# Kernel optimization log

Hardware: AMD Instinct MI355X
Metric: run time of the kernel (lower is better)

Reference implementation:

```python
import jax, jax.numpy as jnp
import numpy as np

NUM_IMU = 72
NUM_NOISE = 12
MAX_PROP = 300
LN_EPS = 1e-5

def _softplus(x):
    return jax.nn.softplus(x)

def setup_inputs() -> dict:
    key = jax.random.key(0)
    k1, k2, k3, k4, k5 = jax.random.split(key, 5)
    d_model = 1024
    seq_len = 4096
    hidden_states = jax.random.normal(k1, (1, seq_len, d_model), dtype=jnp.float32)
    ln_gamma = jnp.ones((d_model,), dtype=jnp.float32)
    ln_beta = jnp.zeros((d_model,), dtype=jnp.float32)
    # Linear: d_model -> NUM_IMU * NUM_NOISE
    W = jax.random.normal(k2, (d_model, NUM_IMU * NUM_NOISE), dtype=jnp.float32) / np.sqrt(d_model)
    b = jax.random.normal(k3, (NUM_IMU * NUM_NOISE,), dtype=jnp.float32) * 0.01
    return {"hidden_states": hidden_states, "ln_gamma": ln_gamma, "ln_beta": ln_beta, "W": W, "b": b}

def _forward(hidden_states, ln_gamma, ln_beta, W, b):
    seq_len = hidden_states.shape[1]
    tsteps = min(MAX_PROP, seq_len)
    x = hidden_states[0]  # [seq, d_model] (squeeze batch=1)
    mu = jnp.mean(x, axis=-1, keepdims=True)
    var = jnp.mean((x - mu) ** 2, axis=-1, keepdims=True)
    xn = (x - mu) * jax.lax.rsqrt(var + LN_EPS) * ln_gamma + ln_beta
    # noise params: [seq, NUM_NOISE, NUM_IMU]
    p = (xn @ W + b).reshape(seq_len, NUM_NOISE, NUM_IMU)
    c = p[:, 4, :]
    c_theta = p[:, 5, :]
    phi = p[:, 6, :]
    phi_theta = p[:, 7, :]
    d = _softplus(p[:, 1, :])
    k = d ** 2 / 4 + _softplus(p[:, 0, :])
    d_theta = _softplus(p[:, 3, :])
    k_theta = d_theta ** 2 / 4 + _softplus(p[:, 2, :])
    acc_base = p[:, 8, :].T      # [imu, seq]
    acc_std = _softplus(p[:, 9, :]).T
    gyro_base = p[:, 10, :].T
    gyro_std = _softplus(p[:, 11, :]).T
    # vectorize over imu: move to [imu, seq, 1]
    def I(a):
        return a.T[:, :, None]
    t = jnp.arange(tsteps, dtype=jnp.float32)[None, None, :]  # [1,1,tstep]
    k_, d_, phi_, c_ = I(k), I(d), I(phi), I(c)
    kt_, dt_, pht_, ct_ = I(k_theta), I(d_theta), I(phi_theta), I(c_theta)
    omega1 = jnp.sqrt(k_ * 4 - d_ ** 2) / 2
    lin = c_ * jnp.exp(-d_ / 2 * t) * jnp.sin(t * omega1 + phi_)
    omega2 = jnp.sqrt(kt_ * 4 - dt_ ** 2) / 2
    ang = ct_ * jnp.exp(-dt_ / 2 * t) * jnp.sin(t * omega2 + pht_)
    spring = lin + ang  # [imu, seq, tstep]
    # banded scatter-add: out[s+t] += spring[:, s, t] for s+t < seq_len
    pos = jnp.arange(seq_len, dtype=jnp.int32)[:, None] + jnp.arange(tsteps, dtype=jnp.int32)[None, :]
    pos_flat = pos.reshape(-1)
    mask = pos_flat < seq_len
    pos_safe = jnp.where(mask, pos_flat, 0)
    vals = spring.reshape(NUM_IMU, -1) * mask.astype(spring.dtype)
    kinematics = jnp.zeros((NUM_IMU, seq_len), dtype=spring.dtype).at[:, pos_safe].add(vals)
    return kinematics, acc_base, acc_std, gyro_base, gyro_std

def reference(hidden_states, ln_gamma, ln_beta, W, b):
    return _forward(hidden_states, ln_gamma, ln_beta, W, b)
```

## Files before the change

### kernel.cpp

```cpp
#include <hip/hip_runtime.h>
#include <hip/hip_bf16.h>
#include <math.h>

#define SEQ 4096
#define DM  1024
#define NIMU 72
#define NNOISE 12
#define NJ (NIMU*NNOISE)
#define TSTEPS 300
#define PLANE (NIMU*SEQ)

#define A2F_SHORTS ((size_t)256 * 64 * 512)
#define BTF_SHORTS ((size_t)56 * 64 * 512)

typedef __attribute__((ext_vector_type(8))) short bf16x8;
typedef __attribute__((ext_vector_type(4))) float f32x4;
typedef __attribute__((ext_vector_type(2))) float f32x2;

__device__ __forceinline__ float softplus_f(float x) {
    return fmaxf(x, 0.f) + log1pf(expf(-fabsf(x)));
}

__device__ __forceinline__ void split_bf16(float x, short& hi, short& lo) {
    unsigned b = __float_as_uint(x);
    unsigned h = (b + 0x7FFFu + ((b >> 16) & 1u)) >> 16;
    float hf = __uint_as_float(h << 16);
    float r = x - hf;
    unsigned b2 = __float_as_uint(r);
    unsigned l2 = (b2 + 0x7FFFu + ((b2 >> 16) & 1u)) >> 16;
    hi = (short)h;
    lo = (short)l2;
}

__global__ __launch_bounds__(256) void ln_kernel(const float* __restrict__ x,
                                                 const float* __restrict__ gamma,
                                                 const float* __restrict__ beta,
                                                 short* __restrict__ A2f) {
    const int s_tile = blockIdx.x;
    const int tid = threadIdx.x;
    const int mrow = tid >> 4;
    const int g    = tid & 15;
    const int row  = s_tile * 16 + mrow;
    const float4* xr = (const float4*)(x + (size_t)row * DM);

    float s = 0.f, sq = 0.f;
    #pragma unroll
    for (int i = 0; i < 16; ++i) {
        float4 v = xr[g + 16 * i];
        s  += v.x + v.y + v.z + v.w;
        sq += v.x*v.x + v.y*v.y + v.z*v.z + v.w*v.w;
    }
    #pragma unroll
    for (int off = 1; off < 16; off <<= 1) {
        s  += __shfl_xor(s, off);
        sq += __shfl_xor(sq, off);
    }
    const float mean = s * (1.f / DM);
    const float var  = sq * (1.f / DM) - mean * mean;
    const float rstd = rsqrtf(fmaxf(var, 0.f) + 1e-5f);

    #pragma unroll
    for (int i = 0; i < 16; ++i) {
        float4 v = xr[g + 16 * i];
        float4 gm = ((const float4*)gamma)[g + 16 * i];
        float4 bt = ((const float4*)beta)[g + 16 * i];
        float o[4];
        o[0] = (v.x - mean) * rstd * gm.x + bt.x;
        o[1] = (v.y - mean) * rstd * gm.y + bt.y;
        o[2] = (v.z - mean) * rstd * gm.z + bt.z;
        o[3] = (v.w - mean) * rstd * gm.w + bt.w;
        short4 hv, lv;
        split_bf16(o[0], hv.x, lv.x);
        split_bf16(o[1], hv.y, lv.y);
        split_bf16(o[2], hv.z, lv.z);
        split_bf16(o[3], hv.w, lv.w);
        const int ch = (g >> 3) + 2 * i;
        const size_t base = ((size_t)s_tile * 64 + ch) * 512
                          + mrow * 8 + ((g >> 1) & 3) * 128 + (g & 1) * 4;
        *(short4*)(A2f + base)             = hv;
        *(short4*)(A2f + base + 32 * 512)  = lv;
    }
}

__global__ __launch_bounds__(256) void wprep_kernel(const float* __restrict__ W,
                                                    short* __restrict__ Btf) {
    __shared__ float T[32][33];
    const int k0 = blockIdx.x * 32, j0 = blockIdx.y * 32;
    const int t = threadIdx.x;
    {
        const int r = t >> 3, c4 = (t & 7) * 4;
        float4 v = *(const float4*)(W + (size_t)(k0 + r) * NJ + j0 + c4);
        T[r][c4 + 0] = v.x; T[r][c4 + 1] = v.y; T[r][c4 + 2] = v.z; T[r][c4 + 3] = v.w;
    }
    __syncthreads();
    if (t < 128) {
        const int gq = t >> 6;
        const int l  = t & 63;
        const int n = l & 15, c = l >> 4;
        const int jt = blockIdx.y * 2 + gq;
        bf16x8 hv, lv;
        #pragma unroll
        for (int o = 0; o < 8; ++o) {
            short h, lo_;
            split_bf16(T[c * 8 + o][gq * 16 + n], h, lo_);
            hv[o] = h; lv[o] = lo_;
        }
        short* dh = Btf + ((size_t)jt * 64 + blockIdx.x) * 512 + l * 8;
        *(bf16x8*)dh = hv;
        *(bf16x8*)(dh + (size_t)32 * 512) = lv;
    }
}

__global__ __launch_bounds__(256, 1) void gemm_kernel(const short* __restrict__ A2f,
                                                      const short* __restrict__ Btf,
                                                      const float* __restrict__ bias,
                                                      float* __restrict__ pt) {
    const int l = threadIdx.x & 63, w = threadIdx.x >> 6;
    const int st0 = blockIdx.x * 8 + (w & 1) * 4;
    const int jt0 = blockIdx.y * 8 + (w >> 1) * 4;
    const short* aB = A2f + (size_t)st0 * (64 * 512) + l * 8;
    const short* bB = Btf + (size_t)jt0 * (64 * 512) + l * 8;

    f32x4 acc[4][4] = {};
    bf16x8 ah[2][4], al[2][4], bh[2][4], bl[2][4];

    auto ldstep = [&](int slot, int i) {
        #pragma unroll
        for (int t = 0; t < 4; ++t) {
            ah[slot][t] = *(const bf16x8*)(aB + ((size_t)t * 64 + i) * 512);
            al[slot][t] = *(const bf16x8*)(aB + ((size_t)t * 64 + 32 + i) * 512);
            bh[slot][t] = *(const bf16x8*)(bB + ((size_t)t * 64 + i) * 512);
            bl[slot][t] = *(const bf16x8*)(bB + ((size_t)t * 64 + 32 + i) * 512);
        }
    };

    ldstep(0, 0);
    #pragma unroll 2
    for (int i = 0; i < 32; ++i) {
        const int cur = i & 1;
        if (i + 1 < 32) ldstep(cur ^ 1, i + 1);
        #pragma unroll
        for (int mi = 0; mi < 4; ++mi)
            #pragma unroll
            for (int ni = 0; ni < 4; ++ni)
                acc[mi][ni] = __builtin_amdgcn_mfma_f32_16x16x32_bf16(
                    ah[cur][mi], bh[cur][ni], acc[mi][ni], 0, 0, 0);
        #pragma unroll
        for (int mi = 0; mi < 4; ++mi)
            #pragma unroll
            for (int ni = 0; ni < 4; ++ni)
                acc[mi][ni] = __builtin_amdgcn_mfma_f32_16x16x32_bf16(
                    ah[cur][mi], bl[cur][ni], acc[mi][ni], 0, 0, 0);
        #pragma unroll
        for (int mi = 0; mi < 4; ++mi)
            #pragma unroll
            for (int ni = 0; ni < 4; ++ni)
                acc[mi][ni] = __builtin_amdgcn_mfma_f32_16x16x32_bf16(
                    al[cur][mi], bh[cur][ni], acc[mi][ni], 0, 0, 0);
    }

    const int srow = (l >> 4) * 4;
    const int jcol = l & 15;
    #pragma unroll
    for (int ni = 0; ni < 4; ++ni) {
        const int j = (jt0 + ni) * 16 + jcol;
        if (j < NJ) {
            const float bj = bias[j];
            #pragma unroll
            for (int mi = 0; mi < 4; ++mi) {
                f32x4 v = acc[mi][ni];
                v[0] += bj; v[1] += bj; v[2] += bj; v[3] += bj;
                *(f32x4*)(pt + (size_t)j * SEQ + (st0 + mi) * 16 + srow) = v;
            }
        }
    }
}

__global__ __launch_bounds__(256) void spring_kernel(const float* __restrict__ pt,
                                                     float* __restrict__ kin) {
    __shared__ float win[4 * 368];
    const int tid  = threadIdx.x;
    const int lane = tid & 63;
    const int wid  = tid >> 6;
    const int s0   = blockIdx.x * 256;
    const int imu  = blockIdx.y;
    const int s    = s0 + (wid << 6) + lane;

    float* w0 = win + wid * 368;
    #pragma unroll
    for (int i = 0; i < 6; ++i) {
        const int idx = lane + i * 64;
        if (idx < 363) w0[idx] = 0.f;
    }

    const int base = imu * SEQ + s;
    const float p0  = pt[(size_t)0 * PLANE + base];
    const float p1  = pt[(size_t)1 * PLANE + base];
    const float p2  = pt[(size_t)2 * PLANE + base];
    const float p3  = pt[(size_t)3 * PLANE + base];
    const float c1  = pt[(size_t)4 * PLANE + base];
    const float c2  = pt[(size_t)5 * PLANE + base];
    const float ph1 = pt[(size_t)6 * PLANE + base];
    const float ph2 = pt[(size_t)7 * PLANE + base];

    float dd = softplus_f(p1);
    float kk = dd * dd * 0.25f + softplus_f(p0);
    float om1 = 0.5f * sqrtf(fmaxf(4.f * kk - dd * dd, 0.f));
    float dt = softplus_f(p3);
    float kt = dt * dt * 0.25f + softplus_f(p2);
    float om2 = 0.5f * sqrtf(fmaxf(4.f * kt - dt * dt, 0.f));
    float e1 = expf(-0.5f * dd), e2 = expf(-0.5f * dt);
    float sn, cs, sn2, cs2;
    sincosf(om1, &sn, &cs);
    sincosf(om2, &sn2, &cs2);
    f32x2 Rr = {e1 * cs, e2 * cs2};
    f32x2 Ri = {e1 * sn, e2 * sn2};
    sincosf(ph1, &sn, &cs);
    sincosf(ph2, &sn2, &cs2);
    f32x2 zr = {c1 * cs, c2 * cs2};
    f32x2 zi = {c1 * sn, c2 * sn2};

    f32x2 zrB, ziB;
    {
        f32x2 prr = Rr, pri = Ri;
        f32x2 qr = {1.f, 1.f}, qi = {0.f, 0.f};
        int e = 150;
        while (e) {
            if (e & 1) {
                f32x2 nr = qr * prr - qi * pri;
                qi = qr * pri + qi * prr;
                qr = nr;
            }
            f32x2 nr = prr * prr - pri * pri;
            pri = 2.f * prr * pri;
            prr = nr;
            e >>= 1;
        }
        f32x2 nr = zr * qr - zi * qi;
        ziB = zr * qi + zi * qr;
        zrB = nr;
    }

    float* wp = w0 + lane;
    #pragma unroll 1
    for (int tb = 0; tb < 128; tb += 32) {
        float* wq = wp + tb;
        #pragma unroll
        for (int j = 0; j < 32; ++j) {
            const float vA = zi.x + zi.y;
            const float vB = ziB.x + ziB.y;
            const float a = wq[j];
            const float b = wq[j + 150];
            wq[j]       = a + vA;
            wq[j + 150] = b + vB;
            f32x2 nr = zr * Rr - zi * Ri;
            zi = zr * Ri + zi * Rr;
            zr = nr;
            nr = zrB * Rr - ziB * Ri;
            ziB = zrB * Ri + ziB * Rr;
            zrB = nr;
            __asm__ volatile("" ::: "memory");
        }
    }
    {
        float* wq = wp + 128;
        #pragma unroll
        for (int j = 0; j < 22; ++j) {
            const float vA = zi.x + zi.y;
            const float vB = ziB.x + ziB.y;
            const float a = wq[j];
            const float b = wq[j + 150];
            wq[j]       = a + vA;
            wq[j + 150] = b + vB;
            f32x2 nr = zr * Rr - zi * Ri;
            zi = zr * Ri + zi * Rr;
            zr = nr;
            nr = zrB * Rr - ziB * Ri;
            ziB = zrB * Ri + ziB * Rr;
            zrB = nr;
            __asm__ volatile("" ::: "memory");
        }
    }

    __syncthreads();
    for (int i = tid; i < 555; i += 256) {
        float sum = 0.f;
        #pragma unroll
        for (int w = 0; w < 4; ++w) {
            const int idx = i - (w << 6);
            if (idx >= 0 && idx < 363) sum += win[w * 368 + idx];
        }
        const int pos = s0 + i;
        if (pos < SEQ) {
            (void)__hip_atomic_fetch_add(&kin[(size_t)imu * SEQ + pos], sum,
                                         __ATOMIC_RELAXED, __HIP_MEMORY_SCOPE_AGENT);
        }
    }
}

__global__ __launch_bounds__(256) void tail_kernel(const float* __restrict__ pt,
                                                   float* __restrict__ out) {
    int idx = blockIdx.x * 256 + threadIdx.x;
    if (idx >= 4 * PLANE) return;
    float v = pt[(size_t)8 * PLANE + idx];
    int q = idx / PLANE;
    if (q & 1) v = softplus_f(v);
    out[(size_t)PLANE + idx] = v;
}

extern "C" void kernel_launch(void* const* d_in, const int* in_sizes, int n_in,
                              void* d_out, int out_size, void* d_ws, size_t ws_size,
                              hipStream_t stream) {
    const float* hs    = (const float*)d_in[0];
    const float* gamma = (const float*)d_in[1];
    const float* beta  = (const float*)d_in[2];
    const float* W     = (const float*)d_in[3];
    const float* b     = (const float*)d_in[4];
    float* out = (float*)d_out;

    short* A2f = (short*)d_ws;
    short* Btf = A2f + A2F_SHORTS;
    float* pt  = (float*)(Btf + BTF_SHORTS);

    hipMemsetAsync(out, 0, (size_t)PLANE * sizeof(float), stream);

    ln_kernel<<<SEQ / 16, 256, 0, stream>>>(hs, gamma, beta, A2f);
    wprep_kernel<<<dim3(DM / 32, NJ / 32), 256, 0, stream>>>(W, Btf);
    gemm_kernel<<<dim3(SEQ / 128, 7), 256, 0, stream>>>(A2f, Btf, b, pt);
    spring_kernel<<<dim3(SEQ / 256, NIMU), 256, 0, stream>>>(pt, out);
    tail_kernel<<<(4 * PLANE + 255) / 256, 256, 0, stream>>>(pt, out);
}
```

Baseline: 146.4 us.

## Fuse tail outputs into GEMM epilogue, remap GEMM grid, triple-buffer spring LDS accumulation

The GEMM epilogue now writes noise channels 8-11 (with softplus on the std channels) straight to the output, which removes the separate tail kernel and its pass over pt. The GEMM grid becomes 1D with a swizzled block-to-tile mapping, likely aimed at L2 reuse across XCDs. The spring kernel spreads its LDS read-modify-write accumulation over three shared buffers, so that consecutive timesteps hit independent addresses and break the load/store dependency chain. The cost is triple the LDS zeroing and a three-way sum in the reduction.

```diff
diff --git a/kernel.cpp b/kernel.cpp
--- a/kernel.cpp
+++ b/kernel.cpp
@@ -114,10 +114,16 @@
 __global__ __launch_bounds__(256, 1) void gemm_kernel(const short* __restrict__ A2f,
                                                       const short* __restrict__ Btf,
                                                       const float* __restrict__ bias,
-                                                      float* __restrict__ pt) {
+                                                      float* __restrict__ pt,
+                                                      float* __restrict__ out) {
+    const int bid = blockIdx.x;
+    const int c = bid & 7, k = bid >> 3;
+    const int kd7 = k / 7;
+    const int bx = c * 4 + kd7;
+    const int by = k - kd7 * 7;
     const int l = threadIdx.x & 63, w = threadIdx.x >> 6;
-    const int st0 = blockIdx.x * 8 + (w & 1) * 4;
-    const int jt0 = blockIdx.y * 8 + (w >> 1) * 4;
+    const int st0 = bx * 8 + (w & 1) * 4;
+    const int jt0 = by * 8 + (w >> 1) * 4;
     const short* aB = A2f + (size_t)st0 * (64 * 512) + l * 8;
     const short* bB = Btf + (size_t)jt0 * (64 * 512) + l * 8;
 
@@ -163,14 +169,32 @@
     const int jcol = l & 15;
     #pragma unroll
     for (int ni = 0; ni < 4; ++ni) {
-        const int j = (jt0 + ni) * 16 + jcol;
+        const int jt = jt0 + ni;
+        const int j = jt * 16 + jcol;
         if (j < NJ) {
             const float bj = bias[j];
-            #pragma unroll
-            for (int mi = 0; mi < 4; ++mi) {
-                f32x4 v = acc[mi][ni];
-                v[0] += bj; v[1] += bj; v[2] += bj; v[3] += bj;
-                *(f32x4*)(pt + (size_t)j * SEQ + (st0 + mi) * 16 + srow) = v;
+            if (jt < 36) {
+                #pragma unroll
+                for (int mi = 0; mi < 4; ++mi) {
+                    f32x4 v = acc[mi][ni];
+                    v[0] += bj; v[1] += bj; v[2] += bj; v[3] += bj;
+                    *(f32x4*)(pt + (size_t)j * SEQ + (st0 + mi) * 16 + srow) = v;
+                }
+            } else {
+                const int noise = j / 72;
+                const int imu = j - noise * 72;
+                float* dst = out + (size_t)(noise - 7) * PLANE + (size_t)imu * SEQ;
+                const bool sp = (noise & 1);
+                #pragma unroll
+                for (int mi = 0; mi < 4; ++mi) {
+                    f32x4 v = acc[mi][ni];
+                    v[0] += bj; v[1] += bj; v[2] += bj; v[3] += bj;
+                    if (sp) {
+                        v[0] = softplus_f(v[0]); v[1] = softplus_f(v[1]);
+                        v[2] = softplus_f(v[2]); v[3] = softplus_f(v[3]);
+                    }
+                    *(f32x4*)(dst + (st0 + mi) * 16 + srow) = v;
+                }
             }
         }
     }
@@ -178,7 +202,7 @@
 
 __global__ __launch_bounds__(256) void spring_kernel(const float* __restrict__ pt,
                                                      float* __restrict__ kin) {
-    __shared__ float win[4 * 368];
+    __shared__ float w3[3][4 * 368];
     const int tid  = threadIdx.x;
     const int lane = tid & 63;
     const int wid  = tid >> 6;
@@ -186,12 +210,13 @@
     const int imu  = blockIdx.y;
     const int s    = s0 + (wid << 6) + lane;
 
-    float* w0 = win + wid * 368;
-    #pragma unroll
-    for (int i = 0; i < 6; ++i) {
-        const int idx = lane + i * 64;
-        if (idx < 363) w0[idx] = 0.f;
-    }
+    #pragma unroll
+    for (int b = 0; b < 3; ++b)
+        #pragma unroll
+        for (int i = 0; i < 6; ++i) {
+            const int idx = lane + i * 64;
+            if (idx < 363) w3[b][wid * 368 + idx] = 0.f;
+        }
 
     const int base = imu * SEQ + s;
     const float p0  = pt[(size_t)0 * PLANE + base];
@@ -241,45 +266,32 @@
         zrB = nr;
     }
 
-    float* wp = w0 + lane;
+    float* q0 = &w3[0][wid * 368 + lane];
+    float* q1 = &w3[1][wid * 368 + lane];
+    float* q2 = &w3[2][wid * 368 + lane];
+
     #pragma unroll 1
-    for (int tb = 0; tb < 128; tb += 32) {
-        float* wq = wp + tb;
-        #pragma unroll
-        for (int j = 0; j < 32; ++j) {
-            const float vA = zi.x + zi.y;
-            const float vB = ziB.x + ziB.y;
-            const float a = wq[j];
-            const float b = wq[j + 150];
-            wq[j]       = a + vA;
-            wq[j + 150] = b + vB;
-            f32x2 nr = zr * Rr - zi * Ri;
-            zi = zr * Ri + zi * Rr;
-            zr = nr;
-            nr = zrB * Rr - ziB * Ri;
-            ziB = zrB * Ri + ziB * Rr;
-            zrB = nr;
-            __asm__ volatile("" ::: "memory");
-        }
-    }
-    {
-        float* wq = wp + 128;
-        #pragma unroll
-        for (int j = 0; j < 22; ++j) {
-            const float vA = zi.x + zi.y;
-            const float vB = ziB.x + ziB.y;
-            const float a = wq[j];
-            const float b = wq[j + 150];
-            wq[j]       = a + vA;
-            wq[j + 150] = b + vB;
-            f32x2 nr = zr * Rr - zi * Ri;
-            zi = zr * Ri + zi * Rr;
-            zr = nr;
-            nr = zrB * Rr - ziB * Ri;
-            ziB = zrB * Ri + ziB * Rr;
-            zrB = nr;
-            __asm__ volatile("" ::: "memory");
-        }
+    for (int j = 0; j < 150; j += 3) {
+        float vA0 = zi.x + zi.y;
+        { f32x2 nr = zr * Rr - zi * Ri; zi = zr * Ri + zi * Rr; zr = nr; }
+        float vA1 = zi.x + zi.y;
+        { f32x2 nr = zr * Rr - zi * Ri; zi = zr * Ri + zi * Rr; zr = nr; }
+        float vA2 = zi.x + zi.y;
+        { f32x2 nr = zr * Rr - zi * Ri; zi = zr * Ri + zi * Rr; zr = nr; }
+        float vB0 = ziB.x + ziB.y;
+        { f32x2 nr = zrB * Rr - ziB * Ri; ziB = zrB * Ri + ziB * Rr; zrB = nr; }
+        float vB1 = ziB.x + ziB.y;
+        { f32x2 nr = zrB * Rr - ziB * Ri; ziB = zrB * Ri + ziB * Rr; zrB = nr; }
+        float vB2 = ziB.x + ziB.y;
+        { f32x2 nr = zrB * Rr - ziB * Ri; ziB = zrB * Ri + ziB * Rr; zrB = nr; }
+
+        const float a0 = q0[j],     b0 = q0[j + 150];
+        const float a1 = q1[j + 1], b1 = q1[j + 151];
+        const float a2 = q2[j + 2], b2 = q2[j + 152];
+        q0[j]       = a0 + vA0;  q0[j + 150] = b0 + vB0;
+        q1[j + 1]   = a1 + vA1;  q1[j + 151] = b1 + vB1;
+        q2[j + 2]   = a2 + vA2;  q2[j + 152] = b2 + vB2;
+        __asm__ volatile("" ::: "memory");
     }
 
     __syncthreads();
@@ -288,7 +300,10 @@
         #pragma unroll
         for (int w = 0; w < 4; ++w) {
             const int idx = i - (w << 6);
-            if (idx >= 0 && idx < 363) sum += win[w * 368 + idx];
+            if (idx >= 0 && idx < 363) {
+                const int o = w * 368 + idx;
+                sum += w3[0][o] + w3[1][o] + w3[2][o];
+            }
         }
         const int pos = s0 + i;
         if (pos < SEQ) {
@@ -296,16 +311,6 @@
                                          __ATOMIC_RELAXED, __HIP_MEMORY_SCOPE_AGENT);
         }
     }
-}
-
-__global__ __launch_bounds__(256) void tail_kernel(const float* __restrict__ pt,
-                                                   float* __restrict__ out) {
-    int idx = blockIdx.x * 256 + threadIdx.x;
-    if (idx >= 4 * PLANE) return;
-    float v = pt[(size_t)8 * PLANE + idx];
-    int q = idx / PLANE;
-    if (q & 1) v = softplus_f(v);
-    out[(size_t)PLANE + idx] = v;
 }
 
 extern "C" void kernel_launch(void* const* d_in, const int* in_sizes, int n_in,
@@ -326,7 +331,6 @@
 
     ln_kernel<<<SEQ / 16, 256, 0, stream>>>(hs, gamma, beta, A2f);
     wprep_kernel<<<dim3(DM / 32, NJ / 32), 256, 0, stream>>>(W, Btf);
-    gemm_kernel<<<dim3(SEQ / 128, 7), 256, 0, stream>>>(A2f, Btf, b, pt);
+    gemm_kernel<<<224, 256, 0, stream>>>(A2f, Btf, b, pt, out);
     spring_kernel<<<dim3(SEQ / 256, NIMU), 256, 0, stream>>>(pt, out);
-    tail_kernel<<<(4 * PLANE + 255) / 256, 256, 0, stream>>>(pt, out);
-}
+}
```

Result: slower. 153.8 us (+5.1%).
